# Performance work log

Measured on AMD Instinct MI355X. Metric: run time of the kernel, lower is better.

The kernel has to match this reference:

```python
import jax, jax.numpy as jnp
import numpy as np

D_IN = 1024
D_OUT = 1024


def setup_inputs() -> dict:
    key = jax.random.key(0)
    ks = jax.random.split(key, 7)
    x = jax.random.normal(ks[0], (4, 2048, D_IN), dtype=jnp.float32)
    scale = 1.0 / np.sqrt(D_IN)
    Wq = jax.random.normal(ks[1], (D_IN, D_OUT), dtype=jnp.float32) * scale
    Wk = jax.random.normal(ks[2], (D_IN, D_OUT), dtype=jnp.float32) * scale
    Wv = jax.random.normal(ks[3], (D_IN, D_OUT), dtype=jnp.float32) * scale
    bq = jax.random.normal(ks[4], (D_OUT,), dtype=jnp.float32) * 0.01
    bk = jax.random.normal(ks[5], (D_OUT,), dtype=jnp.float32) * 0.01
    bv = jax.random.normal(ks[6], (D_OUT,), dtype=jnp.float32) * 0.01
    return {"x": x, "Wq": Wq, "bq": bq, "Wk": Wk, "bk": bk, "Wv": Wv, "bv": bv}


def reference(x, Wq, bq, Wk, bk, Wv, bv):
    # x: [B, S, d_in]
    q = jnp.einsum("bsd,de->bse", x, Wq) + bq  # [B, S, d_out]
    k = jnp.einsum("bsd,de->bse", x, Wk) + bk
    v = jnp.einsum("bsd,de->bse", x, Wv) + bv
    d_out = q.shape[-1]
    scores = jnp.einsum("bqe,bke->bqk", q, k) / jnp.sqrt(jnp.float32(d_out))
    attn = jax.nn.softmax(scores, axis=-1)  # [B, S, S]
    return jnp.einsum("bqk,bke->bqe", attn, v)
```

## Files before the change

### kernel.cpp

```cpp
#include <hip/hip_runtime.h>
#include <hip/hip_bf16.h>
#include <stdint.h>

typedef __bf16 bf16x8 __attribute__((ext_vector_type(8)));
typedef __bf16 bf16x4 __attribute__((ext_vector_type(4)));
typedef float f32x4 __attribute__((ext_vector_type(4)));

#define DEV __device__ __forceinline__

DEV void gload_lds16(const void* g, void* l) {
  __builtin_amdgcn_global_load_lds((const __attribute__((address_space(1))) void*)g,
                                   (__attribute__((address_space(3))) void*)l, 16, 0, 0);
}

#define WAITV0 asm volatile("s_waitcnt vmcnt(0)" ::: "memory")
#define MFMA16x16(a, b, c) __builtin_amdgcn_mfma_f32_16x16x32_bf16(a, b, c, 0, 0, 0)

__global__ __launch_bounds__(256) void pack_all_kernel(
    const float* __restrict__ x,
    const float* __restrict__ Wq, const float* __restrict__ bq,
    const float* __restrict__ Wk, const float* __restrict__ bk,
    const float* __restrict__ Wv, const float* __restrict__ bv,
    __bf16* __restrict__ x16, __bf16* __restrict__ Wt, float* __restrict__ bqkv) {
  __shared__ __bf16 T[64][72];
  const int bid = blockIdx.x;
  const int tid = threadIdx.x;
  if (bid < 768) {
    const int w = bid >> 8;
    const float* W = (w == 0) ? Wq : (w == 1) ? Wk : Wv;
    const float scale = (w == 0) ? 0.03125f : 1.0f;
    const int d0 = (bid & 15) * 64;
    const int e0 = ((bid >> 4) & 15) * 64;
    const int r4 = tid >> 4;
    const int c4 = (tid & 15) * 4;
#pragma unroll
    for (int p = 0; p < 4; ++p) {
      int r = r4 + p * 16;
      f32x4 v = *(const f32x4*)(W + (long)(d0 + r) * 1024 + e0 + c4);
      T[r][c4 + 0] = (__bf16)(v[0] * scale);
      T[r][c4 + 1] = (__bf16)(v[1] * scale);
      T[r][c4 + 2] = (__bf16)(v[2] * scale);
      T[r][c4 + 3] = (__bf16)(v[3] * scale);
    }
    __syncthreads();
    const int e4 = tid >> 3;
    const int dd = (tid & 7) * 8;
#pragma unroll
    for (int p = 0; p < 2; ++p) {
      int e = e4 + p * 32;
      bf16x8 ov;
#pragma unroll
      for (int j = 0; j < 8; ++j) ov[j] = T[dd + j][e];
      *(bf16x8*)(Wt + (long)w * 1048576 + (long)(e0 + e) * 1024 + d0 + dd) = ov;
    }
  } else if (bid < 780) {
    int i = (bid - 768) * 256 + tid;
    if (i < 1024) bqkv[i] = bq[i] * 0.03125f;
    else if (i < 2048) bqkv[i] = bk[i - 1024];
    else if (i < 3072) bqkv[i] = bv[i - 2048];
  } else {
    long i = ((long)(bid - 780) * 256 + tid) * 4;
    const long stride = 2048L * 256 * 4;
    for (; i < 8388608L; i += stride) {
      f32x4 v = *(const f32x4*)(x + i);
      bf16x4 b;
      b[0] = (__bf16)v[0]; b[1] = (__bf16)v[1]; b[2] = (__bf16)v[2]; b[3] = (__bf16)v[3];
      *(bf16x4*)(x16 + i) = b;
    }
  }
}

template <int MODE>
__global__ __launch_bounds__(256, 2) void gemm128_kernel(
    const __bf16* __restrict__ A, int lda,
    const __bf16* __restrict__ B, int ldb, long long bBatchStride, int bmShift,
    const float* __restrict__ bias,
    void* __restrict__ C, int ldc,
    __bf16* __restrict__ vt,
    float* __restrict__ rowpart,
    int nTiles, int nt) {
  constexpr int TILEB = 16384;
  __shared__ __attribute__((aligned(128))) char lds[2 * 2 * TILEB];

  const int tid = threadIdx.x;
  const int lane = tid & 63;
  const int wid = tid >> 6;
  const int wm = wid >> 1, wn = wid & 1;
  const int lo = lane & 15, hi = lane >> 4;

  const int cpx = gridDim.x >> 3;
  const int bid = blockIdx.x;
  const int swz = (bid & 7) * cpx + (bid >> 3);
  const int bm = swz / nTiles, bn = swz % nTiles;

  const __bf16* Bb = B + (long long)(bm >> bmShift) * bBatchStride;

  const __bf16* gA[4]; const __bf16* gB[4]; int lA[4];
#pragma unroll
  for (int l = 0; l < 4; ++l) {
    int s = l * 256 + tid, r = s >> 3;
    int c = (s & 7) ^ (r & 7);
    gA[l] = A + (long long)(bm * 128 + r) * lda + c * 8;
    gB[l] = Bb + (long long)(bn * 128 + r) * ldb + c * 8;
    lA[l] = s * 16;
  }

  const int c0 = ((0 * 4 + hi) ^ (lo & 7)) << 4;
  const int c1 = ((1 * 4 + hi) ^ (lo & 7)) << 4;
  const int aBase = (wm * 64 + lo) * 128;
  const int bBase = TILEB + (wn * 64 + lo) * 128;

  f32x4 acc[4][4] = {};

#define STAGE(tt, buf)                                                \
  do {                                                                \
    const long long ko_ = (long long)(tt) * 64;                       \
    char* lb_ = lds + (buf) * (2 * TILEB);                            \
    _Pragma("unroll") for (int l = 0; l < 4; ++l) {                   \
      gload_lds16(gA[l] + ko_, lb_ + lA[l]);                          \
      gload_lds16(gB[l] + ko_, lb_ + TILEB + lA[l]);                  \
    }                                                                 \
  } while (0)

  STAGE(0, 0);
  WAITV0;
  __builtin_amdgcn_s_barrier();
  __builtin_amdgcn_sched_barrier(0);

  for (int t = 0; t < nt; ++t) {
    if (t + 1 < nt) STAGE(t + 1, (t + 1) & 1);
    const char* base = lds + (t & 1) * (2 * TILEB);

    bf16x8 av[4][2], bv[4][2];
#pragma unroll
    for (int f = 0; f < 4; ++f) {
      av[f][0] = *(const bf16x8*)(base + aBase + f * 16 * 128 + c0);
      av[f][1] = *(const bf16x8*)(base + aBase + f * 16 * 128 + c1);
      bv[f][0] = *(const bf16x8*)(base + bBase + f * 16 * 128 + c0);
      bv[f][1] = *(const bf16x8*)(base + bBase + f * 16 * 128 + c1);
    }
#pragma unroll
    for (int mi = 0; mi < 4; ++mi)
#pragma unroll
      for (int ni = 0; ni < 4; ++ni) {
        acc[mi][ni] = MFMA16x16(av[mi][0], bv[ni][0], acc[mi][ni]);
        acc[mi][ni] = MFMA16x16(av[mi][1], bv[ni][1], acc[mi][ni]);
      }

    if (t + 1 < nt) {
      WAITV0;
      __builtin_amdgcn_s_barrier();
      __builtin_amdgcn_sched_barrier(0);
    }
  }
#undef STAGE

  const long long row0 = (long long)bm * 128 + wm * 64 + hi * 4;
  const long long col0 = (long long)bn * 128 + wn * 64 + lo;

  if (MODE == 0) {
    float* Cf = (float*)C;
#pragma unroll
    for (int ni = 0; ni < 4; ++ni) {
      const long long col = col0 + ni * 16;
#pragma unroll
      for (int mi = 0; mi < 4; ++mi)
#pragma unroll
        for (int j = 0; j < 4; ++j)
          Cf[(row0 + mi * 16 + j) * ldc + col] = acc[mi][ni][j];
    }
  } else if (MODE == 2) {
    if (bn < 16) {
      __bf16* Ch = (__bf16*)C;
#pragma unroll
      for (int ni = 0; ni < 4; ++ni) {
        const long long col = col0 + ni * 16;
        const float bvs = bias[col];
#pragma unroll
        for (int mi = 0; mi < 4; ++mi)
#pragma unroll
          for (int j = 0; j < 4; ++j)
            Ch[(row0 + mi * 16 + j) * ldc + col] = (__bf16)(acc[mi][ni][j] + bvs);
      }
    } else {
      const int b = bm >> 4;
      __bf16* vtb = vt + (long long)b * 2097152;
      const int t0 = (bm & 15) * 128 + wm * 64 + hi * 4;
#pragma unroll
      for (int ni = 0; ni < 4; ++ni) {
        const long long e = (long long)(bn - 16) * 128 + wn * 64 + ni * 16 + lo;
        const float bvs = bias[2048 + e];
#pragma unroll
        for (int mi = 0; mi < 4; ++mi) {
          bf16x4 o;
#pragma unroll
          for (int j = 0; j < 4; ++j) o[j] = (__bf16)(acc[mi][ni][j] + bvs);
          *(bf16x4*)(vtb + e * 2048 + t0 + mi * 16) = o;
        }
      }
    }
  } else {
    __bf16* Ch = (__bf16*)C;
    float ps[4][4];
#pragma unroll
    for (int mi = 0; mi < 4; ++mi)
#pragma unroll
      for (int j = 0; j < 4; ++j) {
        float s0 = 0.f;
#pragma unroll
        for (int ni = 0; ni < 4; ++ni) {
          float e = __expf(acc[mi][ni][j]);
          acc[mi][ni][j] = e;
          s0 += e;
        }
        ps[mi][j] = s0;
      }
#pragma unroll
    for (int ni = 0; ni < 4; ++ni) {
      const long long col = col0 + ni * 16;
#pragma unroll
      for (int mi = 0; mi < 4; ++mi)
#pragma unroll
        for (int j = 0; j < 4; ++j)
          Ch[(row0 + mi * 16 + j) * ldc + col] = (__bf16)acc[mi][ni][j];
    }
#pragma unroll
    for (int mi = 0; mi < 4; ++mi)
#pragma unroll
      for (int j = 0; j < 4; ++j) {
        float v = ps[mi][j];
        v += __shfl_xor(v, 1);
        v += __shfl_xor(v, 2);
        v += __shfl_xor(v, 4);
        v += __shfl_xor(v, 8);
        ps[mi][j] = v;
      }
    if (lo == 0) {
      float* rp = rowpart + (long long)(bn * 2 + wn) * 8192;
#pragma unroll
      for (int mi = 0; mi < 4; ++mi) {
        f32x4 o;
#pragma unroll
        for (int j = 0; j < 4; ++j) o[j] = ps[mi][j];
        *(f32x4*)(rp + row0 + mi * 16) = o;
      }
    }
  }
}

__global__ __launch_bounds__(256, 2) void gemm_pv_kernel(
    const __bf16* __restrict__ A, int lda,
    const __bf16* __restrict__ B, int ldb, long long bBatchStride, int bmShift,
    const float* __restrict__ rowpart,
    float* __restrict__ C, int ldc,
    int nTiles, int nt) {
  constexpr int TILEB = 16384;
  __shared__ __attribute__((aligned(128))) char lds[2 * 2 * TILEB];
  __shared__ float rowInvS[128];

  const int tid = threadIdx.x;
  const int lane = tid & 63;
  const int wid = tid >> 6;
  const int wm = wid >> 1, wn = wid & 1;
  const int lo = lane & 15, hi = lane >> 4;

  const int cpx = gridDim.x >> 3;
  const int bid = blockIdx.x;
  const int swz = (bid & 7) * cpx + (bid >> 3);
  const int bm = swz / nTiles, bn = swz % nTiles;

  const __bf16* Bb = B + (long long)(bm >> bmShift) * bBatchStride;

  const __bf16* gA[4]; const __bf16* gB[4]; int lA[4];
#pragma unroll
  for (int l = 0; l < 4; ++l) {
    int s = l * 256 + tid, r = s >> 3;
    int c = (s & 7) ^ (r & 7);
    gA[l] = A + (long long)(bm * 128 + r) * lda + c * 8;
    gB[l] = Bb + (long long)(bn * 128 + r) * ldb + c * 8;
    lA[l] = s * 16;
  }

  const int c0 = ((0 * 4 + hi) ^ (lo & 7)) << 4;
  const int c1 = ((1 * 4 + hi) ^ (lo & 7)) << 4;
  const int aBase = (wm * 64 + lo) * 128;
  const int bBase = TILEB + (wn * 64 + lo) * 128;

  f32x4 acc[4][4] = {};

#define STAGE(tt, buf)                                                \
  do {                                                                \
    const long long ko_ = (long long)(tt) * 64;                       \
    char* lb_ = lds + (buf) * (2 * TILEB);                            \
    _Pragma("unroll") for (int l = 0; l < 4; ++l) {                   \
      gload_lds16(gA[l] + ko_, lb_ + lA[l]);                          \
      gload_lds16(gB[l] + ko_, lb_ + TILEB + lA[l]);                  \
    }                                                                 \
  } while (0)

  STAGE(0, 0);
  if (tid < 128) {
    const float* rp = rowpart + bm * 128 + tid;
    float s = 0.f;
#pragma unroll
    for (int p = 0; p < 32; ++p) s += rp[p * 8192];
    rowInvS[tid] = 1.0f / s;
  }
  __syncthreads();
  __builtin_amdgcn_sched_barrier(0);

  for (int t = 0; t < nt; ++t) {
    if (t + 1 < nt) STAGE(t + 1, (t + 1) & 1);
    const char* base = lds + (t & 1) * (2 * TILEB);
    bf16x8 av[4][2], bv[4][2];
#pragma unroll
    for (int f = 0; f < 4; ++f) {
      av[f][0] = *(const bf16x8*)(base + aBase + f * 16 * 128 + c0);
      av[f][1] = *(const bf16x8*)(base + aBase + f * 16 * 128 + c1);
      bv[f][0] = *(const bf16x8*)(base + bBase + f * 16 * 128 + c0);
      bv[f][1] = *(const bf16x8*)(base + bBase + f * 16 * 128 + c1);
    }
#pragma unroll
    for (int mi = 0; mi < 4; ++mi)
#pragma unroll
      for (int ni = 0; ni < 4; ++ni) {
        acc[mi][ni] = MFMA16x16(av[mi][0], bv[ni][0], acc[mi][ni]);
        acc[mi][ni] = MFMA16x16(av[mi][1], bv[ni][1], acc[mi][ni]);
      }
    if (t + 1 < nt) {
      WAITV0;
      __builtin_amdgcn_s_barrier();
      __builtin_amdgcn_sched_barrier(0);
    }
  }
#undef STAGE

  const long long row0 = (long long)bm * 128 + wm * 64 + hi * 4;
  const long long col0 = (long long)bn * 128 + wn * 64 + lo;
  const int lrow0 = wm * 64 + hi * 4;
#pragma unroll
  for (int mi = 0; mi < 4; ++mi) {
    f32x4 ri = *(const f32x4*)(rowInvS + lrow0 + mi * 16);
#pragma unroll
    for (int ni = 0; ni < 4; ++ni) {
      const long long col = col0 + ni * 16;
#pragma unroll
      for (int j = 0; j < 4; ++j)
        C[(row0 + mi * 16 + j) * ldc + col] = acc[mi][ni][j] * ri[j];
    }
  }
}

extern "C" void kernel_launch(void* const* d_in, const int* in_sizes, int n_in,
                              void* d_out, int out_size, void* d_ws, size_t ws_size,
                              hipStream_t stream) {
  (void)in_sizes; (void)n_in; (void)out_size;
  const float* x  = (const float*)d_in[0];
  const float* Wq = (const float*)d_in[1];
  const float* bq = (const float*)d_in[2];
  const float* Wk = (const float*)d_in[3];
  const float* bk = (const float*)d_in[4];
  const float* Wv = (const float*)d_in[5];
  const float* bv = (const float*)d_in[6];
  float* out = (float*)d_out;
  char* ws = (char*)d_ws;
  if (ws_size < 124825600ULL) return;

  __bf16* x16   = (__bf16*)(ws + 0);
  __bf16* Wt    = (__bf16*)(ws + 16777216);
  float*  bqkv  = (float*)(ws + 23068672);
  __bf16* QKV   = (__bf16*)(ws + 23080960);
  __bf16* Vt    = (__bf16*)(ws + 73412608);
  __bf16* S     = (__bf16*)(ws + 90189824);
  float*  rowpt = (float*)(ws + 123744256);

  pack_all_kernel<<<2828, 256, 0, stream>>>(x, Wq, bq, Wk, bk, Wv, bv, x16, Wt, bqkv);

  gemm128_kernel<2><<<dim3(1536), 256, 0, stream>>>(
      x16, 1024, Wt, 1024, 0LL, 30, bqkv, QKV, 3072, Vt, nullptr, 24, 16);

  gemm128_kernel<3><<<dim3(1024), 256, 0, stream>>>(
      QKV, 3072, QKV + 1024, 3072, 6291456LL, 4, nullptr, S, 2048, nullptr, rowpt, 16, 16);

  gemm_pv_kernel<<<dim3(512), 256, 0, stream>>>(
      S, 2048, Vt, 2048, 2097152LL, 4, rowpt, out, 1024, 8, 32);
}
```

Measured before the change: 161.6 us.

## Load B operand directly from global memory instead of staging through LDS

Both GEMM kernels now stage only the A tile in LDS. Each wave reads its B fragments straight from global memory into registers every k-step. This halves LDS usage and the global-to-LDS copy traffic, which may allow more occupancy. In exchange, B loads are issued synchronously inside the loop with no prefetch, and B data shared between the two wm waves is fetched twice, which can expose global latency.

```diff
diff --git a/kernel.cpp b/kernel.cpp
--- a/kernel.cpp
+++ b/kernel.cpp
@@ -80,7 +80,7 @@
     float* __restrict__ rowpart,
     int nTiles, int nt) {
   constexpr int TILEB = 16384;
-  __shared__ __attribute__((aligned(128))) char lds[2 * 2 * TILEB];
+  __shared__ __attribute__((aligned(128))) char lds[2 * TILEB];
 
   const int tid = threadIdx.x;
   const int lane = tid & 63;
@@ -95,31 +95,30 @@
 
   const __bf16* Bb = B + (long long)(bm >> bmShift) * bBatchStride;
 
-  const __bf16* gA[4]; const __bf16* gB[4]; int lA[4];
+  const __bf16* gA[4]; int lA[4];
 #pragma unroll
   for (int l = 0; l < 4; ++l) {
     int s = l * 256 + tid, r = s >> 3;
     int c = (s & 7) ^ (r & 7);
     gA[l] = A + (long long)(bm * 128 + r) * lda + c * 8;
-    gB[l] = Bb + (long long)(bn * 128 + r) * ldb + c * 8;
     lA[l] = s * 16;
   }
 
   const int c0 = ((0 * 4 + hi) ^ (lo & 7)) << 4;
   const int c1 = ((1 * 4 + hi) ^ (lo & 7)) << 4;
   const int aBase = (wm * 64 + lo) * 128;
-  const int bBase = TILEB + (wn * 64 + lo) * 128;
+
+  const __bf16* bP = Bb + (long long)(bn * 128 + wn * 64 + lo) * ldb + hi * 8;
+  const long long bF = (long long)16 * ldb;
 
   f32x4 acc[4][4] = {};
 
 #define STAGE(tt, buf)                                                \
   do {                                                                \
     const long long ko_ = (long long)(tt) * 64;                       \
-    char* lb_ = lds + (buf) * (2 * TILEB);                            \
-    _Pragma("unroll") for (int l = 0; l < 4; ++l) {                   \
-      gload_lds16(gA[l] + ko_, lb_ + lA[l]);                          \
-      gload_lds16(gB[l] + ko_, lb_ + TILEB + lA[l]);                  \
-    }                                                                 \
+    char* lb_ = lds + (buf) * TILEB;                                  \
+    _Pragma("unroll") for (int l = 0; l < 4; ++l)                     \
+        gload_lds16(gA[l] + ko_, lb_ + lA[l]);                        \
   } while (0)
 
   STAGE(0, 0);
@@ -129,15 +128,19 @@
 
   for (int t = 0; t < nt; ++t) {
     if (t + 1 < nt) STAGE(t + 1, (t + 1) & 1);
-    const char* base = lds + (t & 1) * (2 * TILEB);
+    const char* base = lds + (t & 1) * TILEB;
+    const long long ko = (long long)t * 64;
 
     bf16x8 av[4][2], bv[4][2];
+#pragma unroll
+    for (int f = 0; f < 4; ++f) {
+      bv[f][0] = *(const bf16x8*)(bP + f * bF + ko);
+      bv[f][1] = *(const bf16x8*)(bP + f * bF + ko + 32);
+    }
 #pragma unroll
     for (int f = 0; f < 4; ++f) {
       av[f][0] = *(const bf16x8*)(base + aBase + f * 16 * 128 + c0);
       av[f][1] = *(const bf16x8*)(base + aBase + f * 16 * 128 + c1);
-      bv[f][0] = *(const bf16x8*)(base + bBase + f * 16 * 128 + c0);
-      bv[f][1] = *(const bf16x8*)(base + bBase + f * 16 * 128 + c1);
     }
 #pragma unroll
     for (int mi = 0; mi < 4; ++mi)
@@ -255,7 +258,7 @@
     float* __restrict__ C, int ldc,
     int nTiles, int nt) {
   constexpr int TILEB = 16384;
-  __shared__ __attribute__((aligned(128))) char lds[2 * 2 * TILEB];
+  __shared__ __attribute__((aligned(128))) char lds[2 * TILEB];
   __shared__ float rowInvS[128];
 
   const int tid = threadIdx.x;
@@ -271,31 +274,30 @@
 
   const __bf16* Bb = B + (long long)(bm >> bmShift) * bBatchStride;
 
-  const __bf16* gA[4]; const __bf16* gB[4]; int lA[4];
+  const __bf16* gA[4]; int lA[4];
 #pragma unroll
   for (int l = 0; l < 4; ++l) {
     int s = l * 256 + tid, r = s >> 3;
     int c = (s & 7) ^ (r & 7);
     gA[l] = A + (long long)(bm * 128 + r) * lda + c * 8;
-    gB[l] = Bb + (long long)(bn * 128 + r) * ldb + c * 8;
     lA[l] = s * 16;
   }
 
   const int c0 = ((0 * 4 + hi) ^ (lo & 7)) << 4;
   const int c1 = ((1 * 4 + hi) ^ (lo & 7)) << 4;
   const int aBase = (wm * 64 + lo) * 128;
-  const int bBase = TILEB + (wn * 64 + lo) * 128;
+
+  const __bf16* bP = Bb + (long long)(bn * 128 + wn * 64 + lo) * ldb + hi * 8;
+  const long long bF = (long long)16 * ldb;
 
   f32x4 acc[4][4] = {};
 
 #define STAGE(tt, buf)                                                \
   do {                                                                \
     const long long ko_ = (long long)(tt) * 64;                       \
-    char* lb_ = lds + (buf) * (2 * TILEB);                            \
-    _Pragma("unroll") for (int l = 0; l < 4; ++l) {                   \
-      gload_lds16(gA[l] + ko_, lb_ + lA[l]);                          \
-      gload_lds16(gB[l] + ko_, lb_ + TILEB + lA[l]);                  \
-    }                                                                 \
+    char* lb_ = lds + (buf) * TILEB;                                  \
+    _Pragma("unroll") for (int l = 0; l < 4; ++l)                     \
+        gload_lds16(gA[l] + ko_, lb_ + lA[l]);                        \
   } while (0)
 
   STAGE(0, 0);
@@ -311,14 +313,18 @@
 
   for (int t = 0; t < nt; ++t) {
     if (t + 1 < nt) STAGE(t + 1, (t + 1) & 1);
-    const char* base = lds + (t & 1) * (2 * TILEB);
+    const char* base = lds + (t & 1) * TILEB;
+    const long long ko = (long long)t * 64;
     bf16x8 av[4][2], bv[4][2];
+#pragma unroll
+    for (int f = 0; f < 4; ++f) {
+      bv[f][0] = *(const bf16x8*)(bP + f * bF + ko);
+      bv[f][1] = *(const bf16x8*)(bP + f * bF + ko + 32);
+    }
 #pragma unroll
     for (int f = 0; f < 4; ++f) {
       av[f][0] = *(const bf16x8*)(base + aBase + f * 16 * 128 + c0);
       av[f][1] = *(const bf16x8*)(base + aBase + f * 16 * 128 + c1);
-      bv[f][0] = *(const bf16x8*)(base + bBase + f * 16 * 128 + c0);
-      bv[f][1] = *(const bf16x8*)(base + bBase + f * 16 * 128 + c1);
     }
 #pragma unroll
     for (int mi = 0; mi < 4; ++mi)
```

Result: slower. 275.8 us (+70.7%).
